# Kernel tuning notes

Hardware: AMD Instinct MI355X
Metric: run time of the kernel (lower is better)

The kernel has to match this reference:

```python
import jax, jax.numpy as jnp
import numpy as np
from jax.scipy.linalg import expm

DIM = 1024
N_ROT = 3


def setup_inputs() -> dict:
    key = jax.random.key(0)
    k1, k2 = jax.random.split(key)
    x = jax.random.normal(k1, (4, 4096, DIM), dtype=jnp.float32)
    # raw parameter tensors; skew-symmetrization (as in reset_parameters) done in reference
    generators = jax.random.normal(k2, (N_ROT, DIM, DIM), dtype=jnp.float32) * 0.02
    return {"x": x, "generators": generators}


def reference(x, generators):
    # skew-symmetrize each generator: G <- 0.5*(G - G^T)
    gens = 0.5 * (generators - jnp.swapaxes(generators, -1, -2))
    # sequential rotations: x = x @ expm(G_i) for each of the N_ROT generators
    for i in range(N_ROT):
        rot = expm(gens[i])  # [DIM, DIM] orthogonal rotation
        x = x @ rot
    return x
```

## Files before the change

kernel.cpp:

```cpp
#include <hip/hip_runtime.h>

#define S 1048576
typedef unsigned short u16;
typedef unsigned int u32;
typedef __attribute__((ext_vector_type(8))) short s8v;
typedef __attribute__((ext_vector_type(4))) float f4v;

__device__ __forceinline__ float bf2f(u16 u){
    union { float f; u32 u; } v; v.u = ((u32)u) << 16; return v.f;
}
__device__ __forceinline__ u16 f2bf(float x){
    u32 u = __float_as_uint(x);
    u32 r = (u + 0x7FFFu + ((u >> 16) & 1u)) >> 16;
    return (u16)r;
}
__device__ __forceinline__ void splitf(float x, u16& h, u16& l){
    h = f2bf(x);
    l = f2bf(x - bf2f(h));
}
__device__ __forceinline__ float pairf(const u16* H, const u16* L, size_t off){
    return bf2f(H[off]) + bf2f(L[off]);
}
__device__ __forceinline__ int sidx(int r, int c){ return (r<<6) + (((c) ^ (r&7))<<3); }
__device__ __forceinline__ void gl16(const void* g, void* l){
    __builtin_amdgcn_global_load_lds((const __attribute__((address_space(1))) void*)g,
                                     (__attribute__((address_space(3))) void*)l, 16, 0, 0);
}
__device__ __forceinline__ void xconv1(const float* __restrict__ X, u16* __restrict__ Xh, int u, int t){
    const size_t idx8 = (size_t)u*2048 + (size_t)t*8;
    float4 v0 = *(const float4*)(X+idx8);
    float4 v1 = *(const float4*)(X+idx8+4);
    float xs[8] = {v0.x,v0.y,v0.z,v0.w,v1.x,v1.y,v1.z,v1.w};
    s8v h;
    #pragma unroll
    for (int i = 0; i < 8; ++i) h[i] = (short)f2bf(xs[i]);
    *(s8v*)(Xh+idx8) = h;
}

__global__ __launch_bounds__(256) void pre_k(const float* __restrict__ G, u16* __restrict__ Abase,
                                             const float* __restrict__ X, u16* __restrict__ Xh){
    __shared__ float Gt[64][65];
    const int bid = blockIdx.x;
    const int t = threadIdx.x;
    if (bid >= 768){
        for (int u = bid - 768; u < 8192; u += 1280) xconv1(X, Xh, u, t);
        return;
    }
    const int bx = bid & 15, by = (bid >> 4) & 15, z = bid >> 8;
    const float* Gz = G + (size_t)z*S;
    u16* Ah = Abase + (size_t)z*2*S;
    u16* Al = Ah + S;
    const int row = t >> 2, cq = (t & 3) << 4;
    const int r0 = by << 6, c0 = bx << 6;
    #pragma unroll
    for (int g = 0; g < 4; ++g){
        float4 v = *(const float4*)(Gz + (size_t)(c0+row)*1024 + r0 + cq + g*4);
        Gt[row][cq+g*4+0]=v.x; Gt[row][cq+g*4+1]=v.y; Gt[row][cq+g*4+2]=v.z; Gt[row][cq+g*4+3]=v.w;
    }
    __syncthreads();
    #pragma unroll
    for (int g = 0; g < 2; ++g){
        const float* p = Gz + (size_t)(r0+row)*1024 + c0 + cq + g*8;
        float4 v0 = *(const float4*)(p);
        float4 v1 = *(const float4*)(p+4);
        float xs[8] = {v0.x,v0.y,v0.z,v0.w,v1.x,v1.y,v1.z,v1.w};
        s8v sh, sl;
        #pragma unroll
        for (int i = 0; i < 8; ++i){
            float gt = Gt[cq + g*8 + i][row];
            u16 h,l; splitf(0.5f*(xs[i]-gt), h, l);
            sh[i] = (short)h; sl[i] = (short)l;
        }
        *(s8v*)(Ah + (size_t)(r0+row)*1024 + c0 + cq + g*8) = sh;
        *(s8v*)(Al + (size_t)(r0+row)*1024 + c0 + cq + g*8) = sl;
    }
}

template<int MODE>
__global__ __launch_bounds__(256) void gemm64_k(const u16* __restrict__ Abase, const u16* __restrict__ Btbase,
                                                u16* __restrict__ Cbase,
                                                const u16* __restrict__ Pab, const u16* __restrict__ Pa2b,
                                                u16* __restrict__ O2base, u16* __restrict__ E2t){
    __shared__ u16 lds[3*8192];
    const int t = threadIdx.x;
    const int z = blockIdx.z;
    const int lin = (int)blockIdx.x + ((int)blockIdx.y << 4);
    const int sw = (lin & 7)*32 + (lin >> 3);
    const int bx = sw & 15, by = sw >> 4;
    const u16* Ah = Abase  + (size_t)z*2*S;
    const u16* Bh = Btbase + (size_t)z*2*S; const u16* Bl = Bh + S;
    u16* Ch = Cbase + (size_t)z*2*S;
    const u16* Pah = Pab + (size_t)z*2*S;   const u16* Pal = Pah + S;
    const u16* P2h = Pa2b + (size_t)z*2*S;
    u16* O2h = O2base + (size_t)z*2*S;
    const int brow = by << 6, bcol = bx << 6;
    const int lane = t & 63, w = t >> 6;
    const int wm = (w >> 1) << 5, wn = (w & 1) << 5;
    const int lr = lane & 15, g = lane >> 4;
    int qq[2]; size_t goA[2], goB[2];
    #pragma unroll
    for (int i = 0; i < 2; ++i){
        int q = (((w<<1)+i)<<6) + lane;
        int r = q >> 3, c = lane & 7;
        qq[i] = q << 3;
        goA[i] = (size_t)(brow+r)*1024 + ((c^(r&7))<<3);
        goB[i] = (size_t)(bcol+r)*1024 + ((c^(r&7))<<3);
    }
    auto issue = [&](int kt){
        u16* L = lds + (kt % 3) * 8192;
        const int k0 = kt << 6;
        #pragma unroll
        for (int i = 0; i < 2; ++i){
            gl16(Ah + goA[i] + k0, L + qq[i]);
            gl16(Bh + goB[i] + k0, L + 4096 + qq[i]);
        }
    };
    issue(0); issue(1);
    f4v acc[2][2] = {};
    for (int kt = 0; kt < 16; ++kt){
        if (kt < 15) asm volatile("s_waitcnt vmcnt(4)" ::: "memory");
        else         asm volatile("s_waitcnt vmcnt(0)" ::: "memory");
        __builtin_amdgcn_s_barrier();
        __builtin_amdgcn_sched_barrier(0);
        if (kt < 14) issue(kt + 2);
        const u16* L = lds + (kt % 3) * 8192;
        #pragma unroll
        for (int ks = 0; ks < 2; ++ks){
            const int ch = (ks << 2) + g;
            s8v a_h[2], b_h[2];
            #pragma unroll
            for (int f = 0; f < 2; ++f){
                const int ra = wm+(f<<4)+lr, rb = wn+(f<<4)+lr;
                a_h[f] = *(const s8v*)&L[sidx(ra,ch)];
                b_h[f] = *(const s8v*)&L[4096 + sidx(rb,ch)];
            }
            __builtin_amdgcn_s_setprio(1);
            #pragma unroll
            for (int mf = 0; mf < 2; ++mf)
                #pragma unroll
                for (int nf = 0; nf < 2; ++nf)
                    acc[mf][nf] = __builtin_amdgcn_mfma_f32_16x16x32_bf16(a_h[mf], b_h[nf], acc[mf][nf], 0,0,0);
            __builtin_amdgcn_s_setprio(0);
        }
    }
    const int orr = g << 2;
    u16 hsv[2][2][4];
    #pragma unroll
    for (int mf = 0; mf < 2; ++mf)
        #pragma unroll
        for (int nf = 0; nf < 2; ++nf)
            #pragma unroll
            for (int r = 0; r < 4; ++r){
                const int orow = brow + wm + (mf<<4) + orr + r;
                const int ocol = bcol + wn + (nf<<4) + lr;
                const size_t off = (size_t)orow*1024 + ocol;
                const float av = acc[mf][nf][r];
                if (MODE == 0){
                    Ch[off] = f2bf(av);
                }
                if (MODE == 1){
                    Ch[off] = f2bf(av);
                    float a = pairf(Bh, Bl, off);
                    O2h[off] = f2bf((1.0f/6.0f)*a - (1.0f/24.0f)*av);
                }
                if (MODE == 2){
                    float a  = pairf(Pah, Pal, off);
                    float a2 = bf2f(P2h[off]);
                    float e = a - 0.5f*a2 - av + (orow == ocol ? 1.0f : 0.0f);
                    u16 h = f2bf(e);
                    O2h[off] = h;
                    hsv[mf][nf][r] = h;
                }
            }
    if (MODE == 2 && z == 2){
        u16 (*Tt)[72] = (u16(*)[72])lds;
        __builtin_amdgcn_s_barrier();
        #pragma unroll
        for (int mf = 0; mf < 2; ++mf)
            #pragma unroll
            for (int nf = 0; nf < 2; ++nf)
                #pragma unroll
                for (int r = 0; r < 4; ++r){
                    const int lrow = wm + (mf<<4) + orr + r;
                    const int lcol = wn + (nf<<4) + lr;
                    Tt[lcol][lrow] = hsv[mf][nf][r];
                }
        __builtin_amdgcn_s_barrier();
        const int rr = t >> 2, cc = (t & 3) << 1;
        #pragma unroll
        for (int i = 0; i < 2; ++i){
            s8v v = *(const s8v*)&Tt[rr][(cc+i)<<3];
            *(s8v*)&E2t[(size_t)(bcol+rr)*1024 + brow + ((cc+i)<<3)] = v;
        }
    }
}

__global__ __launch_bounds__(512) void gemm_big3(const u16* __restrict__ Xh, const u16* __restrict__ Rth,
                                                 float* __restrict__ Y){
    __shared__ u16 lds[2][32768];
    const int bid = blockIdx.x;
    const int swz = (bid & 7)*32 + (bid >> 3);
    const int by = swz >> 2, bx = swz & 3;
    const int brow = by << 8, bcol = bx << 8;
    const int t = threadIdx.x;
    const int lane = t & 63, w = t >> 6;
    const int wm = (w >> 2) << 7, wn = (w & 3) << 6;
    const int lr = lane & 15, g = lane >> 4;
    int xq[4]; size_t gx[4], gb[4];
    #pragma unroll
    for (int i = 0; i < 4; ++i){
        int q = (((w<<2)+i)<<6) + lane;
        int r = q >> 3, c = lane & 7;
        xq[i] = q << 3;
        gx[i] = (size_t)(brow+r)*1024 + ((c^(r&7))<<3);
        gb[i] = (size_t)(bcol+r)*1024 + ((c^(r&7))<<3);
    }
    f4v acc[8][4] = {};
    {
        u16* L = lds[0];
        #pragma unroll
        for (int i = 0; i < 4; ++i){
            gl16(Xh  + gx[i], L + xq[i]);
            gl16(Rth + gb[i], L + 16384 + xq[i]);
        }
    }
    int cur = 0;
    for (int kt = 0; kt < 16; ++kt){
        __syncthreads();
        if (kt < 15){
            u16* L = lds[cur^1];
            const int k0 = (kt+1) << 6;
            #pragma unroll
            for (int i = 0; i < 4; ++i){
                gl16(Xh  + gx[i] + k0, L + xq[i]);
                gl16(Rth + gb[i] + k0, L + 16384 + xq[i]);
            }
        }
        const u16* L = lds[cur];
        #pragma unroll
        for (int ks = 0; ks < 2; ++ks){
            const int ch = (ks << 2) + g;
            s8v bh[4];
            #pragma unroll
            for (int nf = 0; nf < 4; ++nf){
                const int rb = wn+(nf<<4)+lr;
                bh[nf] = *(const s8v*)&L[16384 + sidx(rb,ch)];
            }
            __builtin_amdgcn_s_setprio(1);
            #pragma unroll
            for (int mf = 0; mf < 8; ++mf){
                const int ra = wm+(mf<<4)+lr;
                s8v a = *(const s8v*)&L[sidx(ra,ch)];
                #pragma unroll
                for (int nf = 0; nf < 4; ++nf)
                    acc[mf][nf] = __builtin_amdgcn_mfma_f32_16x16x32_bf16(a, bh[nf], acc[mf][nf], 0,0,0);
            }
            __builtin_amdgcn_s_setprio(0);
        }
        cur ^= 1;
    }
    const int orr = g << 2;
    #pragma unroll
    for (int mf = 0; mf < 8; ++mf)
        #pragma unroll
        for (int nf = 0; nf < 4; ++nf)
            #pragma unroll
            for (int r = 0; r < 4; ++r){
                int orow = brow + wm + (mf<<4) + orr + r;
                int ocol = bcol + wn + (nf<<4) + lr;
                Y[(size_t)orow*1024 + ocol] = acc[mf][nf][r];
            }
}

__global__ __launch_bounds__(512) void gemm_big3x(const float* __restrict__ X, const u16* __restrict__ Rth,
                                                  float* __restrict__ Y){
    __shared__ u16 lds[2*32768];
    const int bid = blockIdx.x;
    const int swz = (bid & 7)*32 + (bid >> 3);
    const int by = swz >> 2, bx = swz & 3;
    const int brow = by << 8, bcol = bx << 8;
    const int t = threadIdx.x;
    const int lane = t & 63, w = t >> 6;
    const int wm = (w >> 2) << 7, wn = (w & 3) << 6;
    const int lr = lane & 15, g = lane >> 4;
    int bq[4]; size_t gb[4];
    #pragma unroll
    for (int i = 0; i < 4; ++i){
        int q = (((w<<2)+i)<<6) + lane;
        int r = q >> 3, c = lane & 7;
        bq[i] = q << 3;
        gb[i] = (size_t)(bcol+r)*1024 + ((c^(r&7))<<3);
    }
    int xrow[4], xc[4];
    #pragma unroll
    for (int i = 0; i < 4; ++i){ int q = (i<<9) + t; xrow[i] = q >> 3; xc[i] = q & 7; }
    auto issueB = [&](int kt){
        u16* L = lds + ((kt & 1) << 15) + 16384;
        const int k0 = kt << 6;
        #pragma unroll
        for (int i = 0; i < 4; ++i) gl16(Rth + gb[i] + k0, L + bq[i]);
    };
    float4 xf[4][2];
    auto loadX = [&](int kt){
        const int k0 = kt << 6;
        #pragma unroll
        for (int i = 0; i < 4; ++i){
            const float* p = X + (size_t)(brow+xrow[i])*1024 + k0 + (xc[i]<<3);
            xf[i][0] = *(const float4*)(p);
            xf[i][1] = *(const float4*)(p+4);
        }
    };
    auto writeX = [&](int kt){
        u16* L = lds + ((kt & 1) << 15);
        #pragma unroll
        for (int i = 0; i < 4; ++i){
            float xs[8] = {xf[i][0].x, xf[i][0].y, xf[i][0].z, xf[i][0].w,
                           xf[i][1].x, xf[i][1].y, xf[i][1].z, xf[i][1].w};
            s8v h;
            #pragma unroll
            for (int j = 0; j < 8; ++j) h[j] = (short)f2bf(xs[j]);
            *(s8v*)&L[sidx(xrow[i], xc[i])] = h;
        }
    };
    f4v acc[8][4] = {};
    loadX(0); issueB(0); writeX(0);
    for (int kt = 0; kt < 16; ++kt){
        __syncthreads();
        if (kt < 15){ loadX(kt + 1); issueB(kt + 1); }
        const u16* L = lds + ((kt & 1) << 15);
        #pragma unroll
        for (int ks = 0; ks < 2; ++ks){
            const int ch = (ks << 2) + g;
            s8v bh[4];
            #pragma unroll
            for (int nf = 0; nf < 4; ++nf){
                const int rb = wn+(nf<<4)+lr;
                bh[nf] = *(const s8v*)&L[16384 + sidx(rb,ch)];
            }
            __builtin_amdgcn_s_setprio(1);
            #pragma unroll
            for (int mf = 0; mf < 8; ++mf){
                const int ra = wm+(mf<<4)+lr;
                s8v a = *(const s8v*)&L[sidx(ra,ch)];
                #pragma unroll
                for (int nf = 0; nf < 4; ++nf)
                    acc[mf][nf] = __builtin_amdgcn_mfma_f32_16x16x32_bf16(a, bh[nf], acc[mf][nf], 0,0,0);
            }
            __builtin_amdgcn_s_setprio(0);
        }
        if (kt < 15) writeX(kt + 1);
    }
    const int orr = g << 2;
    #pragma unroll
    for (int mf = 0; mf < 8; ++mf)
        #pragma unroll
        for (int nf = 0; nf < 4; ++nf)
            #pragma unroll
            for (int r = 0; r < 4; ++r){
                int orow = brow + wm + (mf<<4) + orr + r;
                int ocol = bcol + wn + (nf<<4) + lr;
                Y[(size_t)orow*1024 + ocol] = acc[mf][nf][r];
            }
}

extern "C" void kernel_launch(void* const* d_in, const int* in_sizes, int n_in,
                              void* d_out, int out_size, void* d_ws, size_t ws_size,
                              hipStream_t stream) {
    const float* X = (const float*)d_in[0];
    const float* G = (const float*)d_in[1];
    float* out = (float*)d_out;
    u16* ob = (u16*)d_out;
    auto slot = [&](int i){ return ob + (size_t)i*2*S; };
    u16* RT = (u16*)d_ws;
    u16* Xh = RT + (size_t)2*S;
    const bool ws_ok = ws_size >= (size_t)36*S;

    dim3 b(256);
    pre_k<<<dim3(ws_ok ? 2048 : 768), b, 0, stream>>>(G, slot(0), X, Xh);
    gemm64_k<1><<<dim3(16,16,3), b, 0, stream>>>(slot(0), slot(0), slot(3),
                                                 slot(0), slot(0), slot(6), slot(15));
    gemm64_k<2><<<dim3(16,16,3), b, 0, stream>>>(slot(6), slot(3), slot(14),
                                                 slot(0), slot(3), slot(9), slot(15));
    gemm64_k<0><<<dim3(16,16,1), b, 0, stream>>>(slot(15), slot(10), slot(12),
                                                 slot(0), slot(0), slot(12), slot(15));
    gemm64_k<0><<<dim3(16,16,1), b, 0, stream>>>(slot(12), slot(9), RT,
                                                 slot(0), slot(0), RT, slot(15));
    if (ws_ok)
        gemm_big3<<<dim3(256), dim3(512), 0, stream>>>(Xh, RT, out);
    else
        gemm_big3x<<<dim3(256), dim3(512), 0, stream>>>(X, RT, out);
}
```

Baseline: 107.9 us.

## Drop bf16 low-part split of generators and overlap X conversion with small GEMMs

Removes the hi/lo bf16 split of the skew-symmetric generators, so only the high part is written and the GEMM epilogues read a single bf16 value. The fp32-to-bf16 conversion of X is divided into three chunks, one in the pre-kernel and one in each of the last two 64x64 GEMM launches, where extra blocks do the conversion. This spreads the memory-bound conversion across launches that underuse the GPU. The GEMM block swizzle is disabled in the fused variant. Dropping the low part lowers the precision of the matrix exponential terms.

```diff
diff --git a/kernel.cpp b/kernel.cpp
--- a/kernel.cpp
+++ b/kernel.cpp
@@ -13,13 +13,6 @@
     u32 u = __float_as_uint(x);
     u32 r = (u + 0x7FFFu + ((u >> 16) & 1u)) >> 16;
     return (u16)r;
-}
-__device__ __forceinline__ void splitf(float x, u16& h, u16& l){
-    h = f2bf(x);
-    l = f2bf(x - bf2f(h));
-}
-__device__ __forceinline__ float pairf(const u16* H, const u16* L, size_t off){
-    return bf2f(H[off]) + bf2f(L[off]);
 }
 __device__ __forceinline__ int sidx(int r, int c){ return (r<<6) + (((c) ^ (r&7))<<3); }
 __device__ __forceinline__ void gl16(const void* g, void* l){
@@ -43,13 +36,12 @@
     const int bid = blockIdx.x;
     const int t = threadIdx.x;
     if (bid >= 768){
-        for (int u = bid - 768; u < 8192; u += 1280) xconv1(X, Xh, u, t);
+        for (int u = bid - 768; u < 2731; u += 1280) xconv1(X, Xh, u, t);
         return;
     }
     const int bx = bid & 15, by = (bid >> 4) & 15, z = bid >> 8;
     const float* Gz = G + (size_t)z*S;
     u16* Ah = Abase + (size_t)z*2*S;
-    u16* Al = Ah + S;
     const int row = t >> 2, cq = (t & 3) << 4;
     const int r0 = by << 6, c0 = bx << 6;
     #pragma unroll
@@ -64,33 +56,44 @@
         float4 v0 = *(const float4*)(p);
         float4 v1 = *(const float4*)(p+4);
         float xs[8] = {v0.x,v0.y,v0.z,v0.w,v1.x,v1.y,v1.z,v1.w};
-        s8v sh, sl;
+        s8v sh;
         #pragma unroll
         for (int i = 0; i < 8; ++i){
             float gt = Gt[cq + g*8 + i][row];
-            u16 h,l; splitf(0.5f*(xs[i]-gt), h, l);
-            sh[i] = (short)h; sl[i] = (short)l;
+            sh[i] = (short)f2bf(0.5f*(xs[i]-gt));
         }
         *(s8v*)(Ah + (size_t)(r0+row)*1024 + c0 + cq + g*8) = sh;
-        *(s8v*)(Al + (size_t)(r0+row)*1024 + c0 + cq + g*8) = sl;
-    }
-}
-
-template<int MODE>
+    }
+}
+
+template<int MODE, bool XFUSE>
 __global__ __launch_bounds__(256) void gemm64_k(const u16* __restrict__ Abase, const u16* __restrict__ Btbase,
                                                 u16* __restrict__ Cbase,
                                                 const u16* __restrict__ Pab, const u16* __restrict__ Pa2b,
-                                                u16* __restrict__ O2base, u16* __restrict__ E2t){
+                                                u16* __restrict__ O2base, u16* __restrict__ E2t,
+                                                const float* __restrict__ X, u16* __restrict__ Xh,
+                                                int u0, int u1){
     __shared__ u16 lds[3*8192];
     const int t = threadIdx.x;
+    if (XFUSE && blockIdx.x >= 16){
+        const int nb = (int)gridDim.x - 16;
+        const int e = ((int)(blockIdx.z*gridDim.y + blockIdx.y))*nb + ((int)blockIdx.x - 16);
+        const int E = nb*(int)gridDim.y*(int)gridDim.z;
+        for (int u = u0 + e; u < u1; u += E) xconv1(X, Xh, u, t);
+        return;
+    }
     const int z = blockIdx.z;
-    const int lin = (int)blockIdx.x + ((int)blockIdx.y << 4);
-    const int sw = (lin & 7)*32 + (lin >> 3);
-    const int bx = sw & 15, by = sw >> 4;
+    int bx, by;
+    if (XFUSE){ bx = blockIdx.x; by = blockIdx.y; }
+    else {
+        const int lin = (int)blockIdx.x + ((int)blockIdx.y << 4);
+        const int sw = (lin & 7)*32 + (lin >> 3);
+        bx = sw & 15; by = sw >> 4;
+    }
     const u16* Ah = Abase  + (size_t)z*2*S;
-    const u16* Bh = Btbase + (size_t)z*2*S; const u16* Bl = Bh + S;
+    const u16* Bh = Btbase + (size_t)z*2*S;
     u16* Ch = Cbase + (size_t)z*2*S;
-    const u16* Pah = Pab + (size_t)z*2*S;   const u16* Pal = Pah + S;
+    const u16* Pah = Pab + (size_t)z*2*S;
     const u16* P2h = Pa2b + (size_t)z*2*S;
     u16* O2h = O2base + (size_t)z*2*S;
     const int brow = by << 6, bcol = bx << 6;
@@ -160,11 +163,11 @@
                 }
                 if (MODE == 1){
                     Ch[off] = f2bf(av);
-                    float a = pairf(Bh, Bl, off);
+                    float a = bf2f(Bh[off]);
                     O2h[off] = f2bf((1.0f/6.0f)*a - (1.0f/24.0f)*av);
                 }
                 if (MODE == 2){
-                    float a  = pairf(Pah, Pal, off);
+                    float a  = bf2f(Pah[off]);
                     float a2 = bf2f(P2h[off]);
                     float e = a - 0.5f*a2 - av + (orow == ocol ? 1.0f : 0.0f);
                     u16 h = f2bf(e);
@@ -377,16 +380,27 @@
 
     dim3 b(256);
     pre_k<<<dim3(ws_ok ? 2048 : 768), b, 0, stream>>>(G, slot(0), X, Xh);
-    gemm64_k<1><<<dim3(16,16,3), b, 0, stream>>>(slot(0), slot(0), slot(3),
-                                                 slot(0), slot(0), slot(6), slot(15));
-    gemm64_k<2><<<dim3(16,16,3), b, 0, stream>>>(slot(6), slot(3), slot(14),
-                                                 slot(0), slot(3), slot(9), slot(15));
-    gemm64_k<0><<<dim3(16,16,1), b, 0, stream>>>(slot(15), slot(10), slot(12),
-                                                 slot(0), slot(0), slot(12), slot(15));
-    gemm64_k<0><<<dim3(16,16,1), b, 0, stream>>>(slot(12), slot(9), RT,
-                                                 slot(0), slot(0), RT, slot(15));
-    if (ws_ok)
+    gemm64_k<1,false><<<dim3(16,16,3), b, 0, stream>>>(slot(0), slot(0), slot(3),
+                                                       slot(0), slot(0), slot(6), slot(15),
+                                                       X, Xh, 0, 0);
+    gemm64_k<2,false><<<dim3(16,16,3), b, 0, stream>>>(slot(6), slot(3), slot(14),
+                                                       slot(0), slot(3), slot(9), slot(15),
+                                                       X, Xh, 0, 0);
+    if (ws_ok){
+        gemm64_k<0,true><<<dim3(64,16,1), b, 0, stream>>>(slot(15), slot(10), slot(12),
+                                                          slot(0), slot(0), slot(12), slot(15),
+                                                          X, Xh, 2731, 5462);
+        gemm64_k<0,true><<<dim3(64,16,1), b, 0, stream>>>(slot(12), slot(9), RT,
+                                                          slot(0), slot(0), RT, slot(15),
+                                                          X, Xh, 5462, 8192);
         gemm_big3<<<dim3(256), dim3(512), 0, stream>>>(Xh, RT, out);
-    else
+    } else {
+        gemm64_k<0,false><<<dim3(16,16,1), b, 0, stream>>>(slot(15), slot(10), slot(12),
+                                                           slot(0), slot(0), slot(12), slot(15),
+                                                           X, Xh, 0, 0);
+        gemm64_k<0,false><<<dim3(16,16,1), b, 0, stream>>>(slot(12), slot(9), RT,
+                                                           slot(0), slot(0), RT, slot(15),
+                                                           X, Xh, 0, 0);
         gemm_big3x<<<dim3(256), dim3(512), 0, stream>>>(X, RT, out);
-}
+    }
+}
```

Result: no change. 108.6 us (+0.7%).
